# Kernel tuning notes

Hardware: AMD Instinct MI355X
Metric: run time of the kernel (lower is better)

## Reference

```python
import jax, jax.numpy as jnp
import numpy as np

D_MODEL, D_K, D_V, H, D_FF = 512, 64, 64, 8, 2048
B, N = 8, 1024
LN_EPS = 1e-5


def _layer_norm(x, g, b):
    mu = jnp.mean(x, axis=-1, keepdims=True)
    var = jnp.mean((x - mu) ** 2, axis=-1, keepdims=True)
    return (x - mu) * jax.lax.rsqrt(var + LN_EPS) * g + b


def setup_inputs() -> dict:
    key = jax.random.key(0)
    ks = jax.random.split(key, 16)
    s = 0.02
    return {
        "queries": jax.random.normal(ks[0], (B, N, D_MODEL), jnp.float32),
        "keys": jax.random.normal(ks[1], (B, N, D_MODEL), jnp.float32),
        "values": jax.random.normal(ks[2], (B, N, D_MODEL), jnp.float32),
        "relative_geometry_weights": jax.random.uniform(ks[3], (B, H, N, N), jnp.float32),
        "pos": jax.random.normal(ks[4], (B, N, D_MODEL), jnp.float32),
        "Wq": jax.random.normal(ks[5], (D_MODEL, H * D_K), jnp.float32) * s,
        "bq": jnp.zeros((H * D_K,), jnp.float32),
        "Wk": jax.random.normal(ks[6], (D_MODEL, H * D_K), jnp.float32) * s,
        "bk": jnp.zeros((H * D_K,), jnp.float32),
        "Wv": jax.random.normal(ks[7], (D_MODEL, H * D_V), jnp.float32) * s,
        "bv": jnp.zeros((H * D_V,), jnp.float32),
        "Wo": jax.random.normal(ks[8], (H * D_V, D_MODEL), jnp.float32) * s,
        "bo": jnp.zeros((D_MODEL,), jnp.float32),
        "ln1_g": jnp.ones((D_MODEL,), jnp.float32),
        "ln1_b": jnp.zeros((D_MODEL,), jnp.float32),
        "W1": jax.random.normal(ks[9], (D_MODEL, D_FF), jnp.float32) * s,
        "b1": jnp.zeros((D_FF,), jnp.float32),
        "W2": jax.random.normal(ks[10], (D_FF, D_MODEL), jnp.float32) * s,
        "b2": jnp.zeros((D_MODEL,), jnp.float32),
        "ln2_g": jnp.ones((D_MODEL,), jnp.float32),
        "ln2_b": jnp.zeros((D_MODEL,), jnp.float32),
    }


def reference(queries, keys, values, relative_geometry_weights, pos,
              Wq, bq, Wk, bk, Wv, bv, Wo, bo, ln1_g, ln1_b,
              W1, b1, W2, b2, ln2_g, ln2_b):
    b, n, _ = queries.shape
    # positional injection on q/k only
    q_in = queries + pos
    k_in = keys + pos
    # projections -> [b, h, n, d]
    q = (q_in @ Wq + bq).reshape(b, n, H, D_K).transpose(0, 2, 1, 3)
    k = (k_in @ Wk + bk).reshape(b, n, H, D_K).transpose(0, 2, 1, 3)
    v = (values @ Wv + bv).reshape(b, n, H, D_V).transpose(0, 2, 1, 3)
    # scaled dot-product scores with geometry bias: log(clamp(w_g)) + scores
    att = jnp.einsum('bhqd,bhkd->bhqk', q, k) / jnp.sqrt(jnp.float32(D_K))
    w_mn = jnp.log(jnp.clip(relative_geometry_weights, 1e-6, None)) + att
    w_mn = jax.nn.softmax(w_mn, axis=-1)
    out = jnp.einsum('bhqk,bhkd->bhqd', w_mn, v)  # [b,h,n,d_v]
    out = out.transpose(0, 2, 1, 3).reshape(b, n, H * D_V) @ Wo + bo
    # residual + layernorm (dropout is identity in eval)
    att_out = _layer_norm(queries + out, ln1_g, ln1_b)
    # position-wise FFN with residual + layernorm
    ff = jax.nn.relu(att_out @ W1 + b1) @ W2 + b2
    return _layer_norm(att_out + ff, ln2_g, ln2_b)
```

## Files before the change

### kernel.cpp

```cpp
#include <hip/hip_runtime.h>
#include <hip/hip_bf16.h>
#include <stdint.h>

#define B_   8
#define N_   1024
#define DM   512
#define H_   8
#define DFF  2048
#define ROWS (B_ * N_)
#define QKV_LD (3 * DM)
#define LOG2E 1.4426950408889634f
#define SCL  (0.125f * LOG2E)

typedef __bf16 bf16x8 __attribute__((ext_vector_type(8)));
typedef float  f32x4  __attribute__((ext_vector_type(4)));

__device__ __forceinline__ void gld_lds16(const void* g, void* l) {
  __builtin_amdgcn_global_load_lds((__attribute__((address_space(1))) void*)g,
                                   (__attribute__((address_space(3))) void*)l, 16, 0, 0);
}

__device__ __forceinline__ unsigned short bfb(float x) {
  __bf16 h = (__bf16)x;
  unsigned short u;
  __builtin_memcpy(&u, &h, 2);
  return u;
}

__global__ __launch_bounds__(256) void prep_x(
    const float* __restrict__ q, const float* __restrict__ k,
    const float* __restrict__ v, const float* __restrict__ pos,
    __bf16* __restrict__ xq, __bf16* __restrict__ xk, __bf16* __restrict__ xv) {
  int i = blockIdx.x * 256 + threadIdx.x;
  float4 pv = ((const float4*)pos)[i];
  float4 qv = ((const float4*)q)[i];
  float4 kv = ((const float4*)k)[i];
  float4 vv = ((const float4*)v)[i];
  ushort4 o;
  o.x = bfb(qv.x + pv.x); o.y = bfb(qv.y + pv.y); o.z = bfb(qv.z + pv.z); o.w = bfb(qv.w + pv.w);
  ((ushort4*)xq)[i] = o;
  o.x = bfb(kv.x + pv.x); o.y = bfb(kv.y + pv.y); o.z = bfb(kv.z + pv.z); o.w = bfb(kv.w + pv.w);
  ((ushort4*)xk)[i] = o;
  o.x = bfb(vv.x); o.y = bfb(vv.y); o.z = bfb(vv.z); o.w = bfb(vv.w);
  ((ushort4*)xv)[i] = o;
}

__global__ __launch_bounds__(256) void transpose_all(
    const float* __restrict__ Wq, const float* __restrict__ Wk,
    const float* __restrict__ Wv, const float* __restrict__ Wo,
    const float* __restrict__ W1, const float* __restrict__ W2,
    __bf16* __restrict__ WqkvT, __bf16* __restrict__ WoT,
    __bf16* __restrict__ W1T, __bf16* __restrict__ W2T) {
  __shared__ float tl[32][33];
  int idx = blockIdx.x;
  const float* src; __bf16* dst; int K, N, t;
  if (idx < 768) {
    src = idx < 256 ? Wq : (idx < 512 ? Wk : Wv);
    dst = WqkvT + (size_t)(idx >> 8) * 512 * 512;
    K = 512; N = 512; t = idx & 255;
  } else if (idx < 1024) { src = Wo; dst = WoT;  K = 512;  N = 512;  t = idx - 768; }
  else if (idx < 2048)   { src = W1; dst = W1T;  K = 512;  N = 2048; t = idx - 1024; }
  else                   { src = W2; dst = W2T;  K = 2048; N = 512;  t = idx - 2048; }
  int tiles_n = N >> 5;
  int tn = t & (tiles_n - 1), tk = t / tiles_n;
  int n0 = tn * 32, k0 = tk * 32;
  int x = threadIdx.x & 31, y4 = threadIdx.x >> 5;
  #pragma unroll
  for (int j = y4; j < 32; j += 8) tl[j][x] = src[(size_t)(k0 + j) * N + n0 + x];
  __syncthreads();
  #pragma unroll
  for (int j = y4; j < 32; j += 8)
    dst[(size_t)(n0 + j) * K + k0 + x] = (__bf16)tl[x][j];
}

__global__ __launch_bounds__(256) void transpose_v(
    const __bf16* __restrict__ QKV, __bf16* __restrict__ Vt) {
  __shared__ __bf16 t[32][33];
  int bh = blockIdx.y;
  int b = bh >> 3, h = bh & 7;
  int tn = blockIdx.x >> 1;
  int td = blockIdx.x & 1;
  int x = threadIdx.x & 31, y4 = threadIdx.x >> 5;
  #pragma unroll
  for (int j = y4; j < 32; j += 8)
    t[j][x] = QKV[(size_t)(b * N_ + tn * 32 + j) * QKV_LD + 2 * DM + h * 64 + td * 32 + x];
  __syncthreads();
  #pragma unroll
  for (int j = y4; j < 32; j += 8)
    Vt[(size_t)(bh * 64 + td * 32 + j) * N_ + tn * 32 + x] = t[x][j];
}

template <int EPI, int BN>
__global__ __launch_bounds__(256, 2) void gemm_bt(
    const __bf16* __restrict__ A0, const __bf16* __restrict__ A1, const __bf16* __restrict__ A2,
    const __bf16* __restrict__ BT,
    const float* __restrict__ bias0, const float* __restrict__ bias1, const float* __restrict__ bias2,
    void* __restrict__ Cp, int M, int N, int K, int nsplit) {
  constexpr int NFR = BN / 32;
  constexpr int WCW = BN / 2;
  constexpr int BI  = BN / 32;
  __shared__ __align__(16) __bf16 As[128 * 64];
  __shared__ __align__(16) __bf16 Bs[BN * 64];
  int tid = threadIdx.x, lane = tid & 63;
  int wave = tid >> 6;
  int wr = (wave >> 1) * 64, wc = (wave & 1) * WCW;

  int gx = N / BN;
  int nwg = gridDim.x;
  int cpx = nwg >> 3;
  int swz = (blockIdx.x & 7) * cpx + (blockIdx.x >> 3);
  int bx = swz % gx, by = swz / gx;
  int row0 = by << 7, col0 = bx * BN;

  int asel = col0 / nsplit;
  const __bf16* A = asel == 0 ? A0 : (asel == 1 ? A1 : A2);
  const float* bias = asel == 0 ? bias0 : (asel == 1 ? bias1 : bias2);

  f32x4 acc[4][NFR] = {};

  for (int kt = 0; kt < K; kt += 64) {
    #pragma unroll
    for (int i = 0; i < 4; ++i) {
      int t = i * 256 + tid;
      int r = t >> 3, cL = t & 7;
      int cS = cL ^ (r & 7);
      gld_lds16(A + (size_t)(row0 + r) * K + kt + cS * 8, As + t * 8);
    }
    #pragma unroll
    for (int i = 0; i < BI; ++i) {
      int t = i * 256 + tid;
      int r = t >> 3, cL = t & 7;
      int cS = cL ^ (r & 7);
      gld_lds16(BT + (size_t)(col0 + r) * K + kt + cS * 8, Bs + t * 8);
    }
    __syncthreads();
    #pragma unroll
    for (int ks = 0; ks < 2; ++ks) {
      bf16x8 af[4], bfr[NFR];
      #pragma unroll
      for (int m = 0; m < 4; ++m) {
        int r = wr + m * 16 + (lane & 15);
        int c = (ks * 4 + (lane >> 4)) ^ (r & 7);
        af[m] = *(const bf16x8*)(As + r * 64 + c * 8);
      }
      #pragma unroll
      for (int n = 0; n < NFR; ++n) {
        int r = wc + n * 16 + (lane & 15);
        int c = (ks * 4 + (lane >> 4)) ^ (r & 7);
        bfr[n] = *(const bf16x8*)(Bs + r * 64 + c * 8);
      }
      #pragma unroll
      for (int m = 0; m < 4; ++m)
        #pragma unroll
        for (int n = 0; n < NFR; ++n)
          acc[m][n] = __builtin_amdgcn_mfma_f32_16x16x32_bf16(af[m], bfr[n], acc[m][n], 0, 0, 0);
    }
    __syncthreads();
  }

  int rb = row0 + wr + ((lane >> 4) << 2);
  int cb = col0 + wc + (lane & 15);
  #pragma unroll
  for (int n = 0; n < NFR; ++n) {
    int c = cb + n * 16;
    float bv = bias[c % nsplit];
    #pragma unroll
    for (int m = 0; m < 4; ++m) {
      #pragma unroll
      for (int j = 0; j < 4; ++j) {
        int r = rb + m * 16 + j;
        float v = acc[m][n][j] + bv;
        if (EPI == 1) v = fmaxf(v, 0.f);
        if (EPI == 2) ((float*)Cp)[(size_t)r * N + c] = v;
        else          ((__bf16*)Cp)[(size_t)r * N + c] = (__bf16)v;
      }
    }
  }
}

__global__ __launch_bounds__(256, 3) void attn_kernel(
    const __bf16* __restrict__ QKV, const __bf16* __restrict__ Vt,
    const float* __restrict__ rgw, __bf16* __restrict__ O) {
  __shared__ __align__(16) __bf16 Qs[64 * 64];
  __shared__ __align__(16) __bf16 Ks[64 * 64];
  __shared__ __align__(16) __bf16 Vs[64 * 64];
  __shared__ __align__(16) float  Ws[64 * 64];
  __shared__ __align__(16) __bf16 Ps[4][16 * 64];

  int tid = threadIdx.x, lane = tid & 63, wave = tid >> 6;
  int flat = blockIdx.x;
  int qt = flat & 15, h = (flat >> 4) & 7, b = flat >> 7;
  int q0 = qt * 64;
  const int g = lane >> 4, u = lane & 15;

  #pragma unroll
  for (int i = 0; i < 2; ++i) {
    int t = i * 256 + tid;
    int r = t >> 3, cL = t & 7, cS = cL ^ (r & 7);
    gld_lds16(QKV + (size_t)(b * N_ + q0 + r) * QKV_LD + h * 64 + cS * 8, Qs + t * 8);
  }
  __syncthreads();
  bf16x8 qf[2];
  {
    int r = wave * 16 + u;
    #pragma unroll
    for (int ks = 0; ks < 2; ++ks) {
      int c = (ks * 4 + g) ^ (r & 7);
      qf[ks] = *(const bf16x8*)(Qs + r * 64 + c * 8);
    }
  }

  float l[4] = {0.f, 0.f, 0.f, 0.f};
  f32x4 oacc[4] = {};
  size_t rgw_tile = ((size_t)(b * H_ + h) * N_ + (size_t)q0) * N_;
  __bf16* pw = &Ps[wave][0];

  for (int kt = 0; kt < N_; kt += 64) {
    #pragma unroll
    for (int i = 0; i < 2; ++i) {
      int t = i * 256 + tid;
      int r = t >> 3, cL = t & 7, cS = cL ^ (r & 7);
      gld_lds16(QKV + (size_t)(b * N_ + kt + r) * QKV_LD + DM + h * 64 + cS * 8, Ks + t * 8);
      gld_lds16(Vt + (size_t)((b * H_ + h) * 64 + r) * N_ + kt + cS * 8, Vs + t * 8);
    }
    #pragma unroll
    for (int i = 0; i < 4; ++i) {
      int C = i * 256 + tid;
      int R = C >> 4;
      int cs0 = (C & 15) << 2;
      int gp = (R >> 2) & 3;
      int sc = cs0 ^ (gp << 2) ^ ((gp & 1) << 4);
      gld_lds16(rgw + rgw_tile + (size_t)R * N_ + kt + sc, Ws + C * 4);
    }
    __syncthreads();

    f32x4 s[4] = {};
    #pragma unroll
    for (int ks = 0; ks < 2; ++ks) {
      #pragma unroll
      for (int n = 0; n < 4; ++n) {
        int r = n * 16 + u;
        int c = (ks * 4 + g) ^ (r & 7);
        bf16x8 kf = *(const bf16x8*)(Ks + r * 64 + c * 8);
        s[n] = __builtin_amdgcn_mfma_f32_16x16x32_bf16(qf[ks], kf, s[n], 0, 0, 0);
      }
    }

    float p[4][4];
    #pragma unroll
    for (int n = 0; n < 4; ++n)
      #pragma unroll
      for (int j = 0; j < 4; ++j) {
        int R = wave * 16 + g * 4 + j;
        float w = Ws[R * 64 + ((n * 16 + u) ^ (g << 2) ^ ((g & 1) << 4))];
        p[n][j] = fmaxf(w, 1e-6f) * exp2f(s[n][j] * SCL);
        l[j] += p[n][j];
      }

    #pragma unroll
    for (int n = 0; n < 4; ++n)
      #pragma unroll
      for (int j = 0; j < 4; ++j) {
        int r = g * 4 + j;
        int col = n * 16 + u;
        int cS = (col >> 3) ^ (r & 7);
        pw[r * 64 + cS * 8 + (col & 7)] = (__bf16)p[n][j];
      }

    #pragma unroll
    for (int ks = 0; ks < 2; ++ks) {
      int cp = (ks * 4 + g) ^ (u & 7);
      bf16x8 pa = *(const bf16x8*)(pw + u * 64 + cp * 8);
      #pragma unroll
      for (int n = 0; n < 4; ++n) {
        int r = n * 16 + u;
        int c = (ks * 4 + g) ^ (r & 7);
        bf16x8 vb = *(const bf16x8*)(Vs + r * 64 + c * 8);
        oacc[n] = __builtin_amdgcn_mfma_f32_16x16x32_bf16(pa, vb, oacc[n], 0, 0, 0);
      }
    }
    __syncthreads();
  }

  #pragma unroll
  for (int o = 1; o < 16; o <<= 1)
    #pragma unroll
    for (int j = 0; j < 4; ++j) l[j] += __shfl_xor(l[j], o);

  int orow = b * N_ + q0 + wave * 16 + g * 4;
  int ocol = h * 64 + u;
  #pragma unroll
  for (int j = 0; j < 4; ++j) {
    float inv = 1.f / l[j];
    #pragma unroll
    for (int n = 0; n < 4; ++n)
      O[(size_t)(orow + j) * DM + ocol + n * 16] = (__bf16)(oacc[n][j] * inv);
  }
}

template <int WRITE_BF>
__global__ __launch_bounds__(256) void ln_kernel(
    const float* __restrict__ x1, const float* __restrict__ x2,
    const float* __restrict__ gw, const float* __restrict__ bw,
    float* __restrict__ outf, __bf16* __restrict__ outb) {
  __shared__ float red[8];
  int row = blockIdx.x, t = threadIdx.x;
  size_t base = (size_t)row * DM;
  float v0 = x1[base + t] + x2[base + t];
  float v1 = x1[base + t + 256] + x2[base + t + 256];
  float s = v0 + v1, s2 = v0 * v0 + v1 * v1;
  #pragma unroll
  for (int o = 32; o; o >>= 1) { s += __shfl_xor(s, o); s2 += __shfl_xor(s2, o); }
  int wave = t >> 6;
  if ((t & 63) == 0) { red[wave] = s; red[4 + wave] = s2; }
  __syncthreads();
  s = red[0] + red[1] + red[2] + red[3];
  s2 = red[4] + red[5] + red[6] + red[7];
  float mu = s * (1.f / DM);
  float var = s2 * (1.f / DM) - mu * mu;
  float rstd = rsqrtf(var + 1e-5f);
  float y0 = (v0 - mu) * rstd * gw[t] + bw[t];
  float y1 = (v1 - mu) * rstd * gw[t + 256] + bw[t + 256];
  outf[base + t] = y0;
  outf[base + t + 256] = y1;
  if (WRITE_BF) {
    outb[base + t] = (__bf16)y0;
    outb[base + t + 256] = (__bf16)y1;
  }
}

extern "C" void kernel_launch(void* const* d_in, const int* in_sizes, int n_in,
                              void* d_out, int out_size, void* d_ws, size_t ws_size,
                              hipStream_t stream) {
  const float* queries = (const float*)d_in[0];
  const float* keys    = (const float*)d_in[1];
  const float* values  = (const float*)d_in[2];
  const float* rgw     = (const float*)d_in[3];
  const float* pos     = (const float*)d_in[4];
  const float* Wq = (const float*)d_in[5];
  const float* bq = (const float*)d_in[6];
  const float* Wk = (const float*)d_in[7];
  const float* bk = (const float*)d_in[8];
  const float* Wv = (const float*)d_in[9];
  const float* bv = (const float*)d_in[10];
  const float* Wo = (const float*)d_in[11];
  const float* bo = (const float*)d_in[12];
  const float* ln1g = (const float*)d_in[13];
  const float* ln1b = (const float*)d_in[14];
  const float* W1 = (const float*)d_in[15];
  const float* b1 = (const float*)d_in[16];
  const float* W2 = (const float*)d_in[17];
  const float* b2 = (const float*)d_in[18];
  const float* ln2g = (const float*)d_in[19];
  const float* ln2b = (const float*)d_in[20];
  float* out = (float*)d_out;

  char* ws = (char*)d_ws;
  const size_t SZX = (size_t)ROWS * DM * 2;
  __bf16* Xq    = (__bf16*)(ws);
  __bf16* Xk    = (__bf16*)(ws + SZX);
  __bf16* Xv    = (__bf16*)(ws + 2 * SZX);
  __bf16* WqkvT = (__bf16*)(ws + 3 * SZX);
  __bf16* WoT   = (__bf16*)(ws + 3 * SZX + 1572864);
  __bf16* W1T   = (__bf16*)(ws + 3 * SZX + 2097152);
  __bf16* W2T   = (__bf16*)(ws + 3 * SZX + 4194304);
  __bf16* QKV   = (__bf16*)(ws + 3 * SZX + 6291456);
  __bf16* Vt    = (__bf16*)(ws + 3 * SZX + 6291456 + 3 * SZX);
  __bf16* Oat   = (__bf16*)(ws + 3 * SZX + 6291456 + 4 * SZX);
  __bf16* ff1   = (__bf16*)(ws + 3 * SZX + 6291456 + 5 * SZX);
  float*  attproj = (float*)Xq;
  __bf16* attoutb = Xv;
  float*  attoutf = (float*)QKV;
  float*  ff2     = (float*)Vt;

  prep_x<<<ROWS * DM / 4 / 256, 256, 0, stream>>>(queries, keys, values, pos, Xq, Xk, Xv);
  transpose_all<<<3072, 256, 0, stream>>>(Wq, Wk, Wv, Wo, W1, W2, WqkvT, WoT, W1T, W2T);

  gemm_bt<0, 128><<<(ROWS / 128) * (QKV_LD / 128), 256, 0, stream>>>(
      Xq, Xk, Xv, WqkvT, bq, bk, bv, QKV, ROWS, QKV_LD, DM, DM);

  transpose_v<<<dim3(64, B_ * H_), 256, 0, stream>>>(QKV, Vt);

  attn_kernel<<<B_ * H_ * (N_ / 64), 256, 0, stream>>>(QKV, Vt, rgw, Oat);

  gemm_bt<2, 64><<<(ROWS / 128) * (DM / 64), 256, 0, stream>>>(
      Oat, Oat, Oat, WoT, bo, bo, bo, attproj, ROWS, DM, DM, DM);

  ln_kernel<1><<<ROWS, 256, 0, stream>>>(queries, attproj, ln1g, ln1b, attoutf, attoutb);

  gemm_bt<1, 128><<<(ROWS / 128) * (DFF / 128), 256, 0, stream>>>(
      attoutb, attoutb, attoutb, W1T, b1, b1, b1, ff1, ROWS, DFF, DM, DFF);

  gemm_bt<2, 64><<<(ROWS / 128) * (DM / 64), 256, 0, stream>>>(
      ff1, ff1, ff1, W2T, b2, b2, b2, ff2, ROWS, DM, DFF, DM);

  ln_kernel<0><<<ROWS, 256, 0, stream>>>(attoutf, ff2, ln2g, ln2b, out, nullptr);
}
```

Baseline: 248.8 us.

## Prefetch geometry weights into registers and double-buffer across attention tiles

```diff
diff --git a/kernel.cpp b/kernel.cpp
--- a/kernel.cpp
+++ b/kernel.cpp
@@ -178,20 +178,22 @@
   }
 }
 
-__global__ __launch_bounds__(256, 3) void attn_kernel(
+__global__ __launch_bounds__(256, 4) void attn_kernel(
     const __bf16* __restrict__ QKV, const __bf16* __restrict__ Vt,
     const float* __restrict__ rgw, __bf16* __restrict__ O) {
   __shared__ __align__(16) __bf16 Qs[64 * 64];
   __shared__ __align__(16) __bf16 Ks[64 * 64];
   __shared__ __align__(16) __bf16 Vs[64 * 64];
-  __shared__ __align__(16) float  Ws[64 * 64];
   __shared__ __align__(16) __bf16 Ps[4][16 * 64];
 
   int tid = threadIdx.x, lane = tid & 63, wave = tid >> 6;
-  int flat = blockIdx.x;
+  int flat = (blockIdx.x & 7) * 128 + (blockIdx.x >> 3);
   int qt = flat & 15, h = (flat >> 4) & 7, b = flat >> 7;
   int q0 = qt * 64;
   const int g = lane >> 4, u = lane & 15;
+
+  const float* rgw_p = rgw +
+      ((size_t)(b * H_ + h) * N_ + (size_t)(q0 + wave * 16 + g * 4)) * N_ + u;
 
   #pragma unroll
   for (int i = 0; i < 2; ++i) {
@@ -199,88 +201,97 @@
     int r = t >> 3, cL = t & 7, cS = cL ^ (r & 7);
     gld_lds16(QKV + (size_t)(b * N_ + q0 + r) * QKV_LD + h * 64 + cS * 8, Qs + t * 8);
   }
-  __syncthreads();
-  bf16x8 qf[2];
-  {
-    int r = wave * 16 + u;
-    #pragma unroll
-    for (int ks = 0; ks < 2; ++ks) {
-      int c = (ks * 4 + g) ^ (r & 7);
-      qf[ks] = *(const bf16x8*)(Qs + r * 64 + c * 8);
-    }
-  }
+  float wA[16], wB[16];
+  #pragma unroll
+  for (int n = 0; n < 4; ++n)
+    #pragma unroll
+    for (int j = 0; j < 4; ++j)
+      wA[n * 4 + j] = rgw_p[(size_t)j * N_ + n * 16];
 
   float l[4] = {0.f, 0.f, 0.f, 0.f};
   f32x4 oacc[4] = {};
-  size_t rgw_tile = ((size_t)(b * H_ + h) * N_ + (size_t)q0) * N_;
+  bf16x8 qf[2];
   __bf16* pw = &Ps[wave][0];
 
-  for (int kt = 0; kt < N_; kt += 64) {
-    #pragma unroll
-    for (int i = 0; i < 2; ++i) {
-      int t = i * 256 + tid;
-      int r = t >> 3, cL = t & 7, cS = cL ^ (r & 7);
-      gld_lds16(QKV + (size_t)(b * N_ + kt + r) * QKV_LD + DM + h * 64 + cS * 8, Ks + t * 8);
-      gld_lds16(Vt + (size_t)((b * H_ + h) * 64 + r) * N_ + kt + cS * 8, Vs + t * 8);
+#define ATTN_TILE(T16, WC, WN, WAIT)                                           \
+  {                                                                            \
+    __syncthreads();                \
+    _Pragma("unroll")                                                          \
+    for (int i = 0; i < 2; ++i) {                                              \
+      int t = i * 256 + tid;                                                   \
+      int r = t >> 3, cL = t & 7, cS = cL ^ (r & 7);                           \
+      gld_lds16(QKV + (size_t)(b * N_ + (T16) * 64 + r) * QKV_LD + DM + h * 64 + cS * 8, Ks + t * 8); \
+      gld_lds16(Vt + (size_t)((b * H_ + h) * 64 + r) * N_ + (T16) * 64 + cS * 8, Vs + t * 8);         \
+    }                                                                          \
+    __builtin_amdgcn_sched_barrier(0);  \
+    if ((T16) < 15) {                                                          \
+      _Pragma("unroll")                                                        \
+      for (int n = 0; n < 4; ++n)                                              \
+        _Pragma("unroll")                                                      \
+        for (int j = 0; j < 4; ++j)                                            \
+          WN[n * 4 + j] = rgw_p[(size_t)j * N_ + ((T16) + 1) * 64 + n * 16];   \
+    }                                                                          \
+    asm volatile(WAIT ::: "memory");                                           \
+    __builtin_amdgcn_s_barrier();                                              \
+    if ((T16) == 0) {                                                          \
+      int r = wave * 16 + u;                                                   \
+      _Pragma("unroll")                                                        \
+      for (int ks = 0; ks < 2; ++ks) {                                         \
+        int c = (ks * 4 + g) ^ (r & 7);                                        \
+        qf[ks] = *(const bf16x8*)(Qs + r * 64 + c * 8);                        \
+      }                                                                        \
+    }                                                                          \
+    f32x4 s[4] = {};                                                           \
+    __builtin_amdgcn_s_setprio(1);                                             \
+    _Pragma("unroll")                                                          \
+    for (int ks = 0; ks < 2; ++ks) {                                           \
+      _Pragma("unroll")                                                        \
+      for (int n = 0; n < 4; ++n) {                                            \
+        int r = n * 16 + u;                                                    \
+        int c = (ks * 4 + g) ^ (r & 7);                                        \
+        bf16x8 kf = *(const bf16x8*)(Ks + r * 64 + c * 8);                     \
+        s[n] = __builtin_amdgcn_mfma_f32_16x16x32_bf16(qf[ks], kf, s[n], 0, 0, 0); \
+      }                                                                        \
+    }                                                                          \
+    __builtin_amdgcn_s_setprio(0);                                             \
+    _Pragma("unroll")                                                          \
+    for (int n = 0; n < 4; ++n)                                                \
+      _Pragma("unroll")                                                        \
+      for (int j = 0; j < 4; ++j) {                                            \
+        float pv = fmaxf(WC[n * 4 + j], 1e-6f) * exp2f(s[n][j] * SCL);         \
+        l[j] += pv;                                                            \
+        int rr = g * 4 + j;                                                    \
+        int col = n * 16 + u;                                                  \
+        int cS2 = (col >> 3) ^ (rr & 7);                                       \
+        pw[rr * 64 + cS2 * 8 + (col & 7)] = (__bf16)pv;                        \
+      }                                                                        \
+    __builtin_amdgcn_s_setprio(1);                                             \
+    _Pragma("unroll")                                                          \
+    for (int ks = 0; ks < 2; ++ks) {                                           \
+      int cp = (ks * 4 + g) ^ (u & 7);                                         \
+      bf16x8 pa = *(const bf16x8*)(pw + u * 64 + cp * 8);                      \
+      _Pragma("unroll")                                                        \
+      for (int n = 0; n < 4; ++n) {                                            \
+        int r = n * 16 + u;                                                    \
+        int c = (ks * 4 + g) ^ (r & 7);                                        \
+        bf16x8 vb = *(const bf16x8*)(Vs + r * 64 + c * 8);                     \
+        oacc[n] = __builtin_amdgcn_mfma_f32_16x16x32_bf16(pa, vb, oacc[n], 0, 0, 0); \
+      }                                                                        \
+    }                                                                          \
+    __builtin_amdgcn_s_setprio(0);                                             \
+  }
+
+  #pragma unroll 1
+  for (int tt = 0; tt < 8; ++tt) {
+    int t2 = tt * 2;
+    ATTN_TILE(t2, wA, wB, "s_waitcnt vmcnt(16)")
+    if (tt < 7) {
+      ATTN_TILE((t2 + 1), wB, wA, "s_waitcnt vmcnt(16)")
+    } else {
+      ATTN_TILE((t2 + 1), wB, wA, "s_waitcnt vmcnt(0)")
     }
-    #pragma unroll
-    for (int i = 0; i < 4; ++i) {
-      int C = i * 256 + tid;
-      int R = C >> 4;
-      int cs0 = (C & 15) << 2;
-      int gp = (R >> 2) & 3;
-      int sc = cs0 ^ (gp << 2) ^ ((gp & 1) << 4);
-      gld_lds16(rgw + rgw_tile + (size_t)R * N_ + kt + sc, Ws + C * 4);
-    }
-    __syncthreads();
-
-    f32x4 s[4] = {};
-    #pragma unroll
-    for (int ks = 0; ks < 2; ++ks) {
-      #pragma unroll
-      for (int n = 0; n < 4; ++n) {
-        int r = n * 16 + u;
-        int c = (ks * 4 + g) ^ (r & 7);
-        bf16x8 kf = *(const bf16x8*)(Ks + r * 64 + c * 8);
-        s[n] = __builtin_amdgcn_mfma_f32_16x16x32_bf16(qf[ks], kf, s[n], 0, 0, 0);
-      }
-    }
-
-    float p[4][4];
-    #pragma unroll
-    for (int n = 0; n < 4; ++n)
-      #pragma unroll
-      for (int j = 0; j < 4; ++j) {
-        int R = wave * 16 + g * 4 + j;
-        float w = Ws[R * 64 + ((n * 16 + u) ^ (g << 2) ^ ((g & 1) << 4))];
-        p[n][j] = fmaxf(w, 1e-6f) * exp2f(s[n][j] * SCL);
-        l[j] += p[n][j];
-      }
-
-    #pragma unroll
-    for (int n = 0; n < 4; ++n)
-      #pragma unroll
-      for (int j = 0; j < 4; ++j) {
-        int r = g * 4 + j;
-        int col = n * 16 + u;
-        int cS = (col >> 3) ^ (r & 7);
-        pw[r * 64 + cS * 8 + (col & 7)] = (__bf16)p[n][j];
-      }
-
-    #pragma unroll
-    for (int ks = 0; ks < 2; ++ks) {
-      int cp = (ks * 4 + g) ^ (u & 7);
-      bf16x8 pa = *(const bf16x8*)(pw + u * 64 + cp * 8);
-      #pragma unroll
-      for (int n = 0; n < 4; ++n) {
-        int r = n * 16 + u;
-        int c = (ks * 4 + g) ^ (r & 7);
-        bf16x8 vb = *(const bf16x8*)(Vs + r * 64 + c * 8);
-        oacc[n] = __builtin_amdgcn_mfma_f32_16x16x32_bf16(pa, vb, oacc[n], 0, 0, 0);
-      }
-    }
-    __syncthreads();
-  }
+  }
+#undef ATTN_TILE
 
   #pragma unroll
   for (int o = 1; o < 16; o <<= 1)
```

Result: slower. 288.8 us (+16.1%).
